# Performance work log

Hardware: AMD Instinct MI355X
Metric: run time of the kernel (lower is better)

## Reference

```python
import jax, jax.numpy as jnp
import numpy as np

N_NODES = 50000


def _gcn_conv(x, W, b, row, col, n):
    # GCNConv (PyG defaults): h = x @ W; add self-loops; symmetric deg normalization; scatter-add; + bias
    h = x @ W
    loops = jnp.arange(n, dtype=row.dtype)
    r = jnp.concatenate([row, loops])
    c = jnp.concatenate([col, loops])
    deg = jax.ops.segment_sum(jnp.ones(r.shape[0], dtype=h.dtype), c, num_segments=n)
    dinv = jnp.where(deg > 0, jax.lax.rsqrt(deg), 0.0)
    norm = dinv[r] * dinv[c]  # [E+n]
    msgs = h[r] * norm[:, None]  # gather + scale
    out = jax.ops.segment_sum(msgs, c, num_segments=n)  # scatter-add to targets
    return out + b


def setup_inputs() -> dict:
    key = jax.random.key(0)
    k1, k2, k3, k4 = jax.random.split(key, 4)
    f_in, hid, f_out = 256, 512, 250
    n, e = N_NODES, 1600000
    x = jax.random.normal(k1, (n, f_in), dtype=jnp.float32)
    edge_index = jax.random.randint(k2, (2, e), 0, n, dtype=jnp.int32)
    W1 = jax.random.normal(k3, (f_in, hid), dtype=jnp.float32) * (1.0 / np.sqrt(f_in))
    b1 = jnp.zeros((hid,), dtype=jnp.float32)
    W2 = jax.random.normal(k4, (hid, f_out), dtype=jnp.float32) * (1.0 / np.sqrt(hid))
    b2 = jnp.zeros((f_out,), dtype=jnp.float32)
    return {"x": x, "edge_index": edge_index, "W1": W1, "b1": b1, "W2": W2, "b2": b2}


def reference(x, edge_index, W1, b1, W2, b2):
    row, col = edge_index[0], edge_index[1]
    n = x.shape[0]
    h = jax.nn.relu(_gcn_conv(x, W1, b1, row, col, n))
    out = jax.nn.relu(_gcn_conv(h, W2, b2, row, col, n))
    return out
```

## Files before the change

kernel.cpp:

```cpp
#include <hip/hip_runtime.h>
#include <hip/hip_bf16.h>


#define F_IN  256
#define F_HID 512
#define F_OUT 250


__global__ __launch_bounds__(256) void init_kernel(int* cnt, int* cursor, int n) {
    int i = blockIdx.x * 256 + threadIdx.x;
    if (i < n) { cnt[i] = 0; cursor[i] = 0; }
}

__global__ __launch_bounds__(256) void hist_kernel(const int* __restrict__ col, int* cnt, int E) {
    int e = blockIdx.x * 256 + threadIdx.x;
    if (e < E) atomicAdd(&cnt[col[e]], 1);
}

__global__ __launch_bounds__(256) void dinv_kernel(const int* __restrict__ cnt, float* dinv, int n) {
    int i = blockIdx.x * 256 + threadIdx.x;
    if (i < n) dinv[i] = rsqrtf((float)(cnt[i] + 1));
}

__global__ __launch_bounds__(1024) void scan_kernel(const int* __restrict__ cnt, int* rowptr, int n) {
    __shared__ int wsum[16];
    __shared__ int carry_s;
    int t = threadIdx.x;
    int wid = t >> 6, lane = t & 63;
    if (t == 0) carry_s = 0;
    __syncthreads();
    for (int base = 0; base < n; base += 1024) {
        int i = base + t;
        int v = (i < n) ? cnt[i] : 0;
        int s = v;
        #pragma unroll
        for (int off = 1; off < 64; off <<= 1) {
            int u = __shfl_up(s, off, 64);
            if (lane >= off) s += u;
        }
        if (lane == 63) wsum[wid] = s;
        __syncthreads();
        if (wid == 0 && lane < 16) {
            int ws = wsum[lane];
            #pragma unroll
            for (int off = 1; off < 16; off <<= 1) {
                int u = __shfl_up(ws, off, 64);
                if (lane >= off) ws += u;
            }
            wsum[lane] = ws;
        }
        __syncthreads();
        int wbase = (wid == 0) ? 0 : wsum[wid - 1];
        int carry = carry_s;
        if (i < n) rowptr[i] = carry + wbase + s - v;
        __syncthreads();
        if (t == 1023) carry_s = carry + wbase + s;
        __syncthreads();
    }
    if (t == 0) rowptr[n] = carry_s;
}

__global__ __launch_bounds__(256) void fill_kernel(const int* __restrict__ row, const int* __restrict__ col,
                                                   const int* __restrict__ rowptr, int* cursor,
                                                   int* csr, int E) {
    int e = blockIdx.x * 256 + threadIdx.x;
    if (e < E) {
        int c = col[e];
        int p = rowptr[c] + atomicAdd(&cursor[c], 1);
        csr[p] = row[e];
    }
}


template<int F, int LDX, bool BIAS_RELU>
__global__ __launch_bounds__(256) void agg_kernel(const float* __restrict__ X,
                                                  const float* __restrict__ dinv,
                                                  const int* __restrict__ rowptr,
                                                  const int* __restrict__ csr,
                                                  const float* __restrict__ bias,
                                                  float* __restrict__ out, int ldo, int n) {
    int c = blockIdx.x * 4 + (threadIdx.x >> 6);
    if (c >= n) return;
    int l = threadIdx.x & 63;
    int f0 = l * 4;
    float dc = dinv[c];

    float4 acc;
    {
        float4 v = *(const float4*)(X + (size_t)c * LDX + f0);
        acc.x = v.x * dc; acc.y = v.y * dc; acc.z = v.z * dc; acc.w = v.w * dc;
    }
    int beg = rowptr[c], end = rowptr[c + 1];
    #pragma unroll 2
    for (int j = beg; j < end; ++j) {
        int r = csr[j];
        float dr = dinv[r];
        float4 v = *(const float4*)(X + (size_t)r * LDX + f0);
        acc.x += dr * v.x; acc.y += dr * v.y; acc.z += dr * v.z; acc.w += dr * v.w;
    }
    acc.x *= dc; acc.y *= dc; acc.z *= dc; acc.w *= dc;

    float* op = out + (size_t)c * ldo + f0;
    if (BIAS_RELU) {
        float b[4];
        #pragma unroll
        for (int q = 0; q < 4; ++q) b[q] = (f0 + q < F) ? bias[f0 + q] : 0.f;
        acc.x = fmaxf(acc.x + b[0], 0.f);
        acc.y = fmaxf(acc.y + b[1], 0.f);
        acc.z = fmaxf(acc.z + b[2], 0.f);
        acc.w = fmaxf(acc.w + b[3], 0.f);
        if (f0 + 3 < F) {
            ((float2*)op)[0] = make_float2(acc.x, acc.y);
            ((float2*)op)[1] = make_float2(acc.z, acc.w);
        } else {
            float a4[4] = {acc.x, acc.y, acc.z, acc.w};
            #pragma unroll
            for (int q = 0; q < 4; ++q)
                if (f0 + q < F) op[q] = a4[q];
        }
    } else {
        *(float4*)op = acc;
    }
}


template<bool BIAS_RELU, bool BV4>
__global__ __launch_bounds__(256) void gemm_kernel(const float* __restrict__ A,
                                                   const float* __restrict__ B,
                                                   const float* __restrict__ bias,
                                                   float* __restrict__ C,
                                                   int M, int N, int K, int ldc) {
    const int BM = 128, BN = 128, BK = 16;
    __shared__ __align__(16) float As[BK][BM + 4];
    __shared__ __align__(16) float Bs[BK][BN + 4];

    int t = threadIdx.x;
    int row0 = blockIdx.x * BM;
    int col0 = blockIdx.y * BN;
    int tm = t & 15, tn = t >> 4;

    int la_r = t >> 2;
    int la_c = (t & 3) * 4;
    int lb_r = t >> 4;
    int lb_c = (t & 15) * 4;

    float acc[8][8] = {};

    for (int k0 = 0; k0 < K; k0 += BK) {
        #pragma unroll
        for (int h = 0; h < 2; ++h) {
            int r = row0 + la_r + h * 64;
            float4 v = make_float4(0.f, 0.f, 0.f, 0.f);
            if (r < M) v = *(const float4*)&A[(size_t)r * K + k0 + la_c];
            As[la_c + 0][la_r + h * 64] = v.x;
            As[la_c + 1][la_r + h * 64] = v.y;
            As[la_c + 2][la_r + h * 64] = v.z;
            As[la_c + 3][la_r + h * 64] = v.w;
        }
        #pragma unroll
        for (int h = 0; h < 2; ++h) {
            int cc = col0 + lb_c + h * 64;
            const float* bp = &B[(size_t)(k0 + lb_r) * N + cc];
            float v0 = 0.f, v1 = 0.f, v2 = 0.f, v3 = 0.f;
            if (BV4) {
                if (cc + 3 < N) { float4 u = *(const float4*)bp; v0 = u.x; v1 = u.y; v2 = u.z; v3 = u.w; }
            } else {
                if (cc + 1 < N)      { float2 u = *(const float2*)bp;       v0 = u.x; v1 = u.y; }
                else if (cc < N)     { v0 = bp[0]; }
                if (cc + 3 < N)      { float2 u = *(const float2*)(bp + 2); v2 = u.x; v3 = u.y; }
                else if (cc + 2 < N) { v2 = bp[2]; }
            }
            Bs[lb_r][lb_c + h * 64 + 0] = v0;
            Bs[lb_r][lb_c + h * 64 + 1] = v1;
            Bs[lb_r][lb_c + h * 64 + 2] = v2;
            Bs[lb_r][lb_c + h * 64 + 3] = v3;
        }
        __syncthreads();
        #pragma unroll
        for (int k = 0; k < BK; ++k) {
            float4 a0 = *(const float4*)&As[k][tm * 4];
            float4 a1 = *(const float4*)&As[k][tm * 4 + 64];
            float4 b0 = *(const float4*)&Bs[k][tn * 4];
            float4 b1 = *(const float4*)&Bs[k][tn * 4 + 64];
            float a[8] = {a0.x, a0.y, a0.z, a0.w, a1.x, a1.y, a1.z, a1.w};
            float b[8] = {b0.x, b0.y, b0.z, b0.w, b1.x, b1.y, b1.z, b1.w};
            #pragma unroll
            for (int i = 0; i < 8; ++i)
                #pragma unroll
                for (int j = 0; j < 8; ++j)
                    acc[i][j] += a[i] * b[j];
        }
        __syncthreads();
    }

    #pragma unroll
    for (int i = 0; i < 8; ++i) {
        int r = row0 + tm * 4 + (i & 3) + (i >> 2) * 64;
        if (r >= M) continue;
        #pragma unroll
        for (int jh = 0; jh < 2; ++jh) {
            int cc = col0 + tn * 4 + jh * 64;
            if (cc + 3 < N) {
                float4 v;
                float* vp = &v.x;
                #pragma unroll
                for (int q = 0; q < 4; ++q) {
                    float z = acc[i][jh * 4 + q];
                    if (BIAS_RELU) z = fmaxf(z + bias[cc + q], 0.f);
                    vp[q] = z;
                }
                *(float4*)&C[(size_t)r * ldc + cc] = v;
            } else {
                #pragma unroll
                for (int q = 0; q < 4; ++q) {
                    if (cc + q < N) {
                        float z = acc[i][jh * 4 + q];
                        if (BIAS_RELU) z = fmaxf(z + bias[cc + q], 0.f);
                        C[(size_t)r * ldc + cc + q] = z;
                    }
                }
            }
        }
    }
}


extern "C" void kernel_launch(void* const* d_in, const int* in_sizes, int n_in,
                              void* d_out, int out_size, void* d_ws, size_t ws_size,
                              hipStream_t stream) {
    const float* x   = (const float*)d_in[0];
    const int*   ei  = (const int*)d_in[1];
    const float* W1  = (const float*)d_in[2];
    const float* b1  = (const float*)d_in[3];
    const float* W2  = (const float*)d_in[4];
    const float* b2  = (const float*)d_in[5];
    float* out = (float*)d_out;

    const int n = in_sizes[0] / F_IN;
    const int E = in_sizes[1] / 2;
    const int* row = ei;
    const int* col = ei + E;

    char* p = (char*)d_ws;
    auto alloc = [&](size_t bytes) { void* r = (void*)p; p += (bytes + 255) & ~(size_t)255; return r; };
    int*   cnt    = (int*)alloc((size_t)n * 4);
    int*   cursor = (int*)alloc((size_t)n * 4);
    int*   rowptr = (int*)alloc((size_t)(n + 1) * 4);
    int*   csr    = (int*)alloc((size_t)E * 4);
    float* dinv   = (float*)alloc((size_t)n * 4);
    float* bufA   = (float*)alloc((size_t)n * 256 * 4);
    float* bufH   = (float*)alloc((size_t)n * F_HID * 4);

    int nb_n = (n + 255) / 256;
    int nb_e = (E + 255) / 256;

    init_kernel<<<nb_n, 256, 0, stream>>>(cnt, cursor, n);
    hist_kernel<<<nb_e, 256, 0, stream>>>(col, cnt, E);
    dinv_kernel<<<nb_n, 256, 0, stream>>>(cnt, dinv, n);
    scan_kernel<<<1, 1024, 0, stream>>>(cnt, rowptr, n);
    fill_kernel<<<nb_e, 256, 0, stream>>>(row, col, rowptr, cursor, csr, E);

    int nb_agg = (n + 3) / 4;

    agg_kernel<F_IN, F_IN, false><<<nb_agg, 256, 0, stream>>>(x, dinv, rowptr, csr, nullptr, bufA, F_IN, n);
    {
        dim3 grid((n + 127) / 128, (F_HID + 127) / 128);
        gemm_kernel<true, true><<<grid, 256, 0, stream>>>(bufA, W1, b1, bufH, n, F_HID, F_IN, F_HID);
    }

    {
        dim3 grid((n + 127) / 128, (F_OUT + 127) / 128);
        gemm_kernel<false, false><<<grid, 256, 0, stream>>>(bufH, W2, nullptr, bufA, n, F_OUT, F_HID, 256);
    }
    agg_kernel<F_OUT, 256, true><<<nb_agg, 256, 0, stream>>>(bufA, dinv, rowptr, csr, b2, out, F_OUT, n);
}
```

Baseline: 1.128 ms.

## Replace FP32 SIMT GEMMs with split-bf16 MFMA GEMMs using hi/lo operand pairs

Both dense GEMMs now run on bf16 MFMA instructions. Each fp32 operand is split into a high and a low bf16 part, and three MFMAs per tile (hi*hi, hi*lo, lo*hi) approximate fp32 accuracy. The aggregation and GEMM1 epilogues write hi/lo bf16 pairs directly, and a new kernel pre-transposes and splits the weights. The aggregation loop unroll also goes from 2 to 4. The aim is to use the matrix cores in place of scalar FMA loops, at the cost of triple MFMA work and some loss of precision.

New measurement: 904.6 us. -19.8%, faster.

```diff
diff --git a/kernel.cpp b/kernel.cpp
--- a/kernel.cpp
+++ b/kernel.cpp
@@ -5,6 +5,18 @@
 #define F_IN  256
 #define F_HID 512
 #define F_OUT 250
+
+using bf16x8 = __attribute__((ext_vector_type(8))) short;
+using f32x4  = __attribute__((ext_vector_type(4))) float;
+
+__device__ __forceinline__ ushort f32_bf16_rne(float f) {
+    uint u = __float_as_uint(f);
+    u += 0x7FFFu + ((u >> 16) & 1u);
+    return (ushort)(u >> 16);
+}
+__device__ __forceinline__ float bf16u_f32(ushort h) {
+    return __uint_as_float(((uint)h) << 16);
+}
 
 
 __global__ __launch_bounds__(256) void init_kernel(int* cnt, int* cursor, int n) {
@@ -72,13 +84,47 @@
 }
 
 
-template<int F, int LDX, bool BIAS_RELU>
+__global__ __launch_bounds__(256) void wsplit_kernel(const float* __restrict__ W,
+                                                     ushort* __restrict__ WThi, ushort* __restrict__ WTlo,
+                                                     int K, int N) {
+    __shared__ float tile[32][33];
+    int t = threadIdx.x;
+    int k0 = blockIdx.x * 32, n0 = blockIdx.y * 32;
+    int r = t >> 3, c = (t & 7) * 4;
+    #pragma unroll
+    for (int q = 0; q < 4; ++q) {
+        float z = 0.f;
+        if (n0 + c + q < N) z = W[(size_t)(k0 + r) * N + n0 + c + q];
+        tile[r][c + q] = z;
+    }
+    __syncthreads();
+    int nr = t >> 3, kq = (t & 7) * 4;
+    int gn = n0 + nr;
+    if (gn < N) {
+        ushort4 h4, l4;
+        ushort* hp = &h4.x; ushort* lp = &l4.x;
+        #pragma unroll
+        for (int q = 0; q < 4; ++q) {
+            float z = tile[kq + q][nr];
+            ushort h = f32_bf16_rne(z);
+            hp[q] = h;
+            lp[q] = f32_bf16_rne(z - bf16u_f32(h));
+        }
+        *(ushort4*)&WThi[(size_t)gn * K + k0 + kq] = h4;
+        *(ushort4*)&WTlo[(size_t)gn * K + k0 + kq] = l4;
+    }
+}
+
+
+template<int F, int LDX, bool BIAS_RELU, bool SPLIT_OUT>
 __global__ __launch_bounds__(256) void agg_kernel(const float* __restrict__ X,
                                                   const float* __restrict__ dinv,
                                                   const int* __restrict__ rowptr,
                                                   const int* __restrict__ csr,
                                                   const float* __restrict__ bias,
-                                                  float* __restrict__ out, int ldo, int n) {
+                                                  float* __restrict__ out,
+                                                  ushort* __restrict__ outHi, ushort* __restrict__ outLo,
+                                                  int ldo, int n) {
     int c = blockIdx.x * 4 + (threadIdx.x >> 6);
     if (c >= n) return;
     int l = threadIdx.x & 63;
@@ -91,7 +137,7 @@
         acc.x = v.x * dc; acc.y = v.y * dc; acc.z = v.z * dc; acc.w = v.w * dc;
     }
     int beg = rowptr[c], end = rowptr[c + 1];
-    #pragma unroll 2
+    #pragma unroll 4
     for (int j = beg; j < end; ++j) {
         int r = csr[j];
         float dr = dinv[r];
@@ -99,6 +145,21 @@
         acc.x += dr * v.x; acc.y += dr * v.y; acc.z += dr * v.z; acc.w += dr * v.w;
     }
     acc.x *= dc; acc.y *= dc; acc.z *= dc; acc.w *= dc;
+
+    if (SPLIT_OUT) {
+        ushort4 h4, l4;
+        float a4[4] = {acc.x, acc.y, acc.z, acc.w};
+        ushort* hp = &h4.x; ushort* lp = &l4.x;
+        #pragma unroll
+        for (int q = 0; q < 4; ++q) {
+            ushort h = f32_bf16_rne(a4[q]);
+            hp[q] = h;
+            lp[q] = f32_bf16_rne(a4[q] - bf16u_f32(h));
+        }
+        *(ushort4*)(outHi + (size_t)c * F + f0) = h4;
+        *(ushort4*)(outLo + (size_t)c * F + f0) = l4;
+        return;
+    }
 
     float* op = out + (size_t)c * ldo + f0;
     if (BIAS_RELU) {
@@ -124,99 +185,107 @@
 }
 
 
-template<bool BIAS_RELU, bool BV4>
-__global__ __launch_bounds__(256) void gemm_kernel(const float* __restrict__ A,
-                                                   const float* __restrict__ B,
-                                                   const float* __restrict__ bias,
-                                                   float* __restrict__ C,
-                                                   int M, int N, int K, int ldc) {
-    const int BM = 128, BN = 128, BK = 16;
-    __shared__ __align__(16) float As[BK][BM + 4];
-    __shared__ __align__(16) float Bs[BK][BN + 4];
+template<bool SPLIT_OUT>
+__global__ __launch_bounds__(256) void gemm_mfma(const ushort* __restrict__ Ahi, const ushort* __restrict__ Alo,
+                                                 const ushort* __restrict__ Bhi, const ushort* __restrict__ Blo,
+                                                 const float* __restrict__ bias,
+                                                 float* __restrict__ Cf,
+                                                 ushort* __restrict__ Chi, ushort* __restrict__ Clo,
+                                                 int M, int N, int K, int ldc) {
+    __shared__ ushort As_hi[128][40];
+    __shared__ ushort As_lo[128][40];
+    __shared__ ushort Bs_hi[128][40];
+    __shared__ ushort Bs_lo[128][40];
 
     int t = threadIdx.x;
-    int row0 = blockIdx.x * BM;
-    int col0 = blockIdx.y * BN;
-    int tm = t & 15, tn = t >> 4;
-
-    int la_r = t >> 2;
-    int la_c = (t & 3) * 4;
-    int lb_r = t >> 4;
-    int lb_c = (t & 15) * 4;
-
-    float acc[8][8] = {};
-
-    for (int k0 = 0; k0 < K; k0 += BK) {
+    int row0 = blockIdx.x * 128;
+    int col0 = blockIdx.y * 128;
+    int lane = t & 63;
+    int w = t >> 6;
+    int wr = w >> 1, wc = w & 1;
+    int lr = lane & 15, lg = lane >> 4;
+
+    int srow = t >> 2;
+    int soct = (t & 3) * 8;
+
+    f32x4 acc[4][4];
+    #pragma unroll
+    for (int i = 0; i < 4; ++i)
+        #pragma unroll
+        for (int j = 0; j < 4; ++j)
+            acc[i][j] = (f32x4){0.f, 0.f, 0.f, 0.f};
+
+    for (int k0 = 0; k0 < K; k0 += 32) {
         #pragma unroll
         for (int h = 0; h < 2; ++h) {
-            int r = row0 + la_r + h * 64;
-            float4 v = make_float4(0.f, 0.f, 0.f, 0.f);
-            if (r < M) v = *(const float4*)&A[(size_t)r * K + k0 + la_c];
-            As[la_c + 0][la_r + h * 64] = v.x;
-            As[la_c + 1][la_r + h * 64] = v.y;
-            As[la_c + 2][la_r + h * 64] = v.z;
-            As[la_c + 3][la_r + h * 64] = v.w;
-        }
-        #pragma unroll
-        for (int h = 0; h < 2; ++h) {
-            int cc = col0 + lb_c + h * 64;
-            const float* bp = &B[(size_t)(k0 + lb_r) * N + cc];
-            float v0 = 0.f, v1 = 0.f, v2 = 0.f, v3 = 0.f;
-            if (BV4) {
-                if (cc + 3 < N) { float4 u = *(const float4*)bp; v0 = u.x; v1 = u.y; v2 = u.z; v3 = u.w; }
+            int r = srow + h * 64;
+            int4 zero = make_int4(0, 0, 0, 0);
+            int ga = row0 + r;
+            int4 vh = zero, vl = zero;
+            if (ga < M) {
+                vh = *(const int4*)(Ahi + (size_t)ga * K + k0 + soct);
+                vl = *(const int4*)(Alo + (size_t)ga * K + k0 + soct);
+            }
+            *(int4*)&As_hi[r][soct] = vh;
+            *(int4*)&As_lo[r][soct] = vl;
+            int gb = col0 + r;
+            int4 wh = zero, wl = zero;
+            if (gb < N) {
+                wh = *(const int4*)(Bhi + (size_t)gb * K + k0 + soct);
+                wl = *(const int4*)(Blo + (size_t)gb * K + k0 + soct);
+            }
+            *(int4*)&Bs_hi[r][soct] = wh;
+            *(int4*)&Bs_lo[r][soct] = wl;
+        }
+        __syncthreads();
+
+        bf16x8 ah[4], al[4], bh[4], bl[4];
+        #pragma unroll
+        for (int mi = 0; mi < 4; ++mi) {
+            ah[mi] = *(const bf16x8*)&As_hi[wr * 64 + mi * 16 + lr][lg * 8];
+            al[mi] = *(const bf16x8*)&As_lo[wr * 64 + mi * 16 + lr][lg * 8];
+        }
+        #pragma unroll
+        for (int ni = 0; ni < 4; ++ni) {
+            bh[ni] = *(const bf16x8*)&Bs_hi[wc * 64 + ni * 16 + lr][lg * 8];
+            bl[ni] = *(const bf16x8*)&Bs_lo[wc * 64 + ni * 16 + lr][lg * 8];
+        }
+        #pragma unroll
+        for (int mi = 0; mi < 4; ++mi)
+            #pragma unroll
+            for (int ni = 0; ni < 4; ++ni) {
+                acc[mi][ni] = __builtin_amdgcn_mfma_f32_16x16x32_bf16(ah[mi], bh[ni], acc[mi][ni], 0, 0, 0);
+                acc[mi][ni] = __builtin_amdgcn_mfma_f32_16x16x32_bf16(ah[mi], bl[ni], acc[mi][ni], 0, 0, 0);
+                acc[mi][ni] = __builtin_amdgcn_mfma_f32_16x16x32_bf16(al[mi], bh[ni], acc[mi][ni], 0, 0, 0);
+            }
+        __syncthreads();
+    }
+
+    #pragma unroll
+    for (int mi = 0; mi < 4; ++mi) {
+        int rbase = row0 + wr * 64 + mi * 16 + lg * 4;
+        #pragma unroll
+        for (int ni = 0; ni < 4; ++ni) {
+            int cg = col0 + wc * 64 + ni * 16 + lr;
+            f32x4 a = acc[mi][ni];
+            if (SPLIT_OUT) {
+                float bia = bias[cg];
+                #pragma unroll
+                for (int r = 0; r < 4; ++r) {
+                    int rg = rbase + r;
+                    if (rg < M) {
+                        float z = fmaxf(a[r] + bia, 0.f);
+                        ushort h = f32_bf16_rne(z);
+                        Chi[(size_t)rg * N + cg] = h;
+                        Clo[(size_t)rg * N + cg] = f32_bf16_rne(z - bf16u_f32(h));
+                    }
+                }
             } else {
-                if (cc + 1 < N)      { float2 u = *(const float2*)bp;       v0 = u.x; v1 = u.y; }
-                else if (cc < N)     { v0 = bp[0]; }
-                if (cc + 3 < N)      { float2 u = *(const float2*)(bp + 2); v2 = u.x; v3 = u.y; }
-                else if (cc + 2 < N) { v2 = bp[2]; }
-            }
-            Bs[lb_r][lb_c + h * 64 + 0] = v0;
-            Bs[lb_r][lb_c + h * 64 + 1] = v1;
-            Bs[lb_r][lb_c + h * 64 + 2] = v2;
-            Bs[lb_r][lb_c + h * 64 + 3] = v3;
-        }
-        __syncthreads();
-        #pragma unroll
-        for (int k = 0; k < BK; ++k) {
-            float4 a0 = *(const float4*)&As[k][tm * 4];
-            float4 a1 = *(const float4*)&As[k][tm * 4 + 64];
-            float4 b0 = *(const float4*)&Bs[k][tn * 4];
-            float4 b1 = *(const float4*)&Bs[k][tn * 4 + 64];
-            float a[8] = {a0.x, a0.y, a0.z, a0.w, a1.x, a1.y, a1.z, a1.w};
-            float b[8] = {b0.x, b0.y, b0.z, b0.w, b1.x, b1.y, b1.z, b1.w};
-            #pragma unroll
-            for (int i = 0; i < 8; ++i)
-                #pragma unroll
-                for (int j = 0; j < 8; ++j)
-                    acc[i][j] += a[i] * b[j];
-        }
-        __syncthreads();
-    }
-
-    #pragma unroll
-    for (int i = 0; i < 8; ++i) {
-        int r = row0 + tm * 4 + (i & 3) + (i >> 2) * 64;
-        if (r >= M) continue;
-        #pragma unroll
-        for (int jh = 0; jh < 2; ++jh) {
-            int cc = col0 + tn * 4 + jh * 64;
-            if (cc + 3 < N) {
-                float4 v;
-                float* vp = &v.x;
-                #pragma unroll
-                for (int q = 0; q < 4; ++q) {
-                    float z = acc[i][jh * 4 + q];
-                    if (BIAS_RELU) z = fmaxf(z + bias[cc + q], 0.f);
-                    vp[q] = z;
-                }
-                *(float4*)&C[(size_t)r * ldc + cc] = v;
-            } else {
-                #pragma unroll
-                for (int q = 0; q < 4; ++q) {
-                    if (cc + q < N) {
-                        float z = acc[i][jh * 4 + q];
-                        if (BIAS_RELU) z = fmaxf(z + bias[cc + q], 0.f);
-                        C[(size_t)r * ldc + cc + q] = z;
+                if (cg < N) {
+                    #pragma unroll
+                    for (int r = 0; r < 4; ++r) {
+                        int rg = rbase + r;
+                        if (rg < M) Cf[(size_t)rg * ldc + cg] = a[r];
                     }
                 }
             }
@@ -243,13 +312,20 @@
 
     char* p = (char*)d_ws;
     auto alloc = [&](size_t bytes) { void* r = (void*)p; p += (bytes + 255) & ~(size_t)255; return r; };
-    int*   cnt    = (int*)alloc((size_t)n * 4);
-    int*   cursor = (int*)alloc((size_t)n * 4);
-    int*   rowptr = (int*)alloc((size_t)(n + 1) * 4);
-    int*   csr    = (int*)alloc((size_t)E * 4);
-    float* dinv   = (float*)alloc((size_t)n * 4);
-    float* bufA   = (float*)alloc((size_t)n * 256 * 4);
-    float* bufH   = (float*)alloc((size_t)n * F_HID * 4);
+    int*    cnt    = (int*)alloc((size_t)n * 4);
+    int*    cursor = (int*)alloc((size_t)n * 4);
+    int*    rowptr = (int*)alloc((size_t)(n + 1) * 4);
+    int*    csr    = (int*)alloc((size_t)E * 4);
+    float*  dinv   = (float*)alloc((size_t)n * 4);
+    ushort* Ahi    = (ushort*)alloc((size_t)n * F_IN * 2);
+    ushort* Alo    = (ushort*)alloc((size_t)n * F_IN * 2);
+    ushort* Hhi    = (ushort*)alloc((size_t)n * F_HID * 2);
+    ushort* Hlo    = (ushort*)alloc((size_t)n * F_HID * 2);
+    ushort* W1Thi  = (ushort*)alloc((size_t)F_HID * F_IN * 2);
+    ushort* W1Tlo  = (ushort*)alloc((size_t)F_HID * F_IN * 2);
+    ushort* W2Thi  = (ushort*)alloc((size_t)F_OUT * F_HID * 2);
+    ushort* W2Tlo  = (ushort*)alloc((size_t)F_OUT * F_HID * 2);
+    float*  bufY   = (float*)Ahi;
 
     int nb_n = (n + 255) / 256;
     int nb_e = (E + 255) / 256;
@@ -260,17 +336,27 @@
     scan_kernel<<<1, 1024, 0, stream>>>(cnt, rowptr, n);
     fill_kernel<<<nb_e, 256, 0, stream>>>(row, col, rowptr, cursor, csr, E);
 
+    {
+        dim3 g1(F_IN / 32, F_HID / 32);
+        wsplit_kernel<<<g1, 256, 0, stream>>>(W1, W1Thi, W1Tlo, F_IN, F_HID);
+        dim3 g2(F_HID / 32, (F_OUT + 31) / 32);
+        wsplit_kernel<<<g2, 256, 0, stream>>>(W2, W2Thi, W2Tlo, F_HID, F_OUT);
+    }
+
     int nb_agg = (n + 3) / 4;
 
-    agg_kernel<F_IN, F_IN, false><<<nb_agg, 256, 0, stream>>>(x, dinv, rowptr, csr, nullptr, bufA, F_IN, n);
+    agg_kernel<F_IN, F_IN, false, true><<<nb_agg, 256, 0, stream>>>(
+        x, dinv, rowptr, csr, nullptr, nullptr, Ahi, Alo, F_IN, n);
     {
-        dim3 grid((n + 127) / 128, (F_HID + 127) / 128);
-        gemm_kernel<true, true><<<grid, 256, 0, stream>>>(bufA, W1, b1, bufH, n, F_HID, F_IN, F_HID);
-    }
-
+        dim3 grid((n + 127) / 128, F_HID / 128);
+        gemm_mfma<true><<<grid, 256, 0, stream>>>(Ahi, Alo, W1Thi, W1Tlo, b1,
+                                                  nullptr, Hhi, Hlo, n, F_HID, F_IN, F_HID);
+    }
     {
         dim3 grid((n + 127) / 128, (F_OUT + 127) / 128);
-        gemm_kernel<false, false><<<grid, 256, 0, stream>>>(bufH, W2, nullptr, bufA, n, F_OUT, F_HID, 256);
-    }
-    agg_kernel<F_OUT, 256, true><<<nb_agg, 256, 0, stream>>>(bufA, dinv, rowptr, csr, b2, out, F_OUT, n);
-}
+        gemm_mfma<false><<<grid, 256, 0, stream>>>(Hhi, Hlo, W2Thi, W2Tlo, nullptr,
+                                                   bufY, nullptr, nullptr, n, F_OUT, F_HID, 256);
+    }
+    agg_kernel<F_OUT, 256, true, false><<<nb_agg, 256, 0, stream>>>(
+        bufY, dinv, rowptr, csr, b2, out, nullptr, nullptr, F_OUT, n);
+}
```
